# Performance work log

Measured on AMD Instinct MI355X. Metric: run time of the kernel, lower is better.

Reference implementation:

```python
import jax, jax.numpy as jnp
import numpy as np

B = 2
N_PER = 100000
M_PER = 27648
C = 32
Z, Y, X = 21, 400, 352
MAX_RANGE = (2, 2, 2)
RADIUS = 8.0
NSAMPLE = 16
VS = np.array([0.2, 0.2, 0.4], np.float32)  # voxel size (x, y, z)


def setup_inputs() -> dict:
    key = jax.random.key(0)
    ks = jax.random.split(key, 6)
    N = B * N_PER
    M = B * M_PER
    space = jnp.array([X * VS[0], Y * VS[1], Z * VS[2]], jnp.float32)
    xyz = jax.random.uniform(ks[0], (N, 3), jnp.float32) * space
    zc = jax.random.randint(ks[1], (M,), 0, Z)
    yc = jax.random.randint(ks[2], (M,), 0, Y)
    xc = jax.random.randint(ks[3], (M,), 0, X)
    bq = jnp.repeat(jnp.arange(B, dtype=jnp.int32), M_PER)
    new_coords = jnp.stack([bq, zc, yc, xc], 1).astype(jnp.int32)
    new_xyz = jnp.stack([(xc + 0.5) * VS[0], (yc + 0.5) * VS[1], (zc + 0.5) * VS[2]], 1).astype(jnp.float32)
    features = jax.random.normal(ks[4], (N, C), jnp.float32)
    raw = jax.random.randint(ks[5], (B, Z, Y, X), -N_PER, N_PER)
    offs = (jnp.arange(B) * N_PER)[:, None, None, None]
    voxel2point_indices = jnp.where(raw < 0, -1, raw + offs).astype(jnp.int32)
    xyz_batch_cnt = jnp.full((B,), N_PER, jnp.int32)
    new_xyz_batch_cnt = jnp.full((B,), M_PER, jnp.int32)
    return dict(new_coords=new_coords, xyz=xyz, xyz_batch_cnt=xyz_batch_cnt,
                new_xyz=new_xyz, new_xyz_batch_cnt=new_xyz_batch_cnt,
                features=features, voxel2point_indices=voxel2point_indices)


def _voxel_query(xyz, new_xyz, new_coords, point_indices):
    """Vectorized equivalent of the CUDA voxel_query kernel.
    Returns (idx (M, nsample) int32 global point indices, empty_ball_mask (M,) bool)."""
    zr, yr, xr = MAX_RANGE
    _, Zg, Yg, Xg = point_indices.shape
    M = new_coords.shape[0]
    dz, dy, dx = jnp.meshgrid(jnp.arange(-zr, zr + 1), jnp.arange(-yr, yr + 1),
                              jnp.arange(-xr, xr + 1), indexing='ij')
    offs = jnp.stack([dz.ravel(), dy.ravel(), dx.ravel()], 1)  # (K,3) in CUDA loop order z,y,x
    nb = new_coords[:, None, 1:4] + offs[None]                 # (M,K,3) candidate voxels
    lim = jnp.array([Zg, Yg, Xg])
    inb = jnp.all((nb >= 0) & (nb < lim), -1)                  # (M,K) in-bounds
    nbc = jnp.clip(nb, 0, lim - 1)
    b = new_coords[:, 0]
    pidx = point_indices[b[:, None], nbc[..., 0], nbc[..., 1], nbc[..., 2]]  # (M,K)
    valid = inb & (pidx >= 0)
    pts = xyz[jnp.maximum(pidx, 0)]                            # (M,K,3)
    d2 = jnp.sum((pts - new_xyz[:, None, :]) ** 2, -1)
    valid = valid & (d2 < RADIUS * RADIUS)
    cnt = jnp.minimum(valid.sum(-1), NSAMPLE)                  # (M,)
    # assign each valid candidate its in-order slot; overflow/invalid go to dump column
    slot = jnp.cumsum(valid, -1) - 1
    slot = jnp.where(valid & (slot < NSAMPLE), slot, NSAMPLE)
    rows = jnp.arange(M)[:, None]
    idx = jnp.zeros((M, NSAMPLE + 1), jnp.int32).at[rows, slot].set(pidx)[:, :NSAMPLE]
    first = idx[:, 0]  # CUDA pre-fills all slots with first found index
    idx = jnp.where(jnp.arange(NSAMPLE)[None, :] < cnt[:, None], idx, first[:, None])
    empty = cnt == 0
    idx = jnp.where(empty[:, None], 0, idx)
    return idx, empty


def reference(new_coords, xyz, xyz_batch_cnt, new_xyz, new_xyz_batch_cnt, features, voxel2point_indices):
    idx, empty = _voxel_query(xyz, new_xyz, new_coords, voxel2point_indices)
    # global -> batch-relative (as in the torch loop), empty balls -> 0 of their batch
    xyz_offs = jnp.concatenate([jnp.zeros(1, jnp.int32), jnp.cumsum(xyz_batch_cnt)[:-1].astype(jnp.int32)])
    qb = new_coords[:, 0]
    idx_rel = jnp.where(empty[:, None], 0, idx - xyz_offs[qb][:, None])
    # grouping_operation (stack version): gather with batch offset added back
    gidx = idx_rel + xyz_offs[qb][:, None]                     # (M, nsample) global indices
    grouped_xyz = jnp.transpose(xyz[gidx], (0, 2, 1))          # (M, 3, nsample)
    grouped_features = jnp.transpose(features[gidx], (0, 2, 1))  # (M, C, nsample)
    return grouped_features, grouped_xyz, empty
```

## Files before the change

kernel.cpp:

```cpp
#include <hip/hip_runtime.h>


constexpr int ZG = 21;
constexpr int YG = 400;
constexpr int XG = 352;
constexpr int NS = 16;
constexpr int CF = 32;
constexpr float R2 = 64.0f;

typedef float v4f __attribute__((ext_vector_type(4)));

__global__ __launch_bounds__(256) void pad_xyz_kernel(
    const float* __restrict__ xyz, float4* __restrict__ xyz4, int N)
{
    const int i = blockIdx.x * 256 + threadIdx.x;
    if (i < N) {
        const float* p = xyz + (size_t)i * 3;
        xyz4[i] = make_float4(p[0], p[1], p[2], 0.0f);
    }
}

template<bool USE4>
__global__ __launch_bounds__(256) void vqg_kernel(
    const int*    __restrict__ new_coords,
    const float*  __restrict__ xyz,
    const float4* __restrict__ xyz4,
    const int*    __restrict__ xyz_batch_cnt,
    const float*  __restrict__ new_xyz,
    const float*  __restrict__ features,
    const int*    __restrict__ v2p,
    float* __restrict__ out_feat,
    float* __restrict__ out_xyz,
    float* __restrict__ out_empty,
    int M)
{
    const int lane = threadIdx.x & 63;
    const int wid  = threadIdx.x >> 6;
    const int m    = blockIdx.x * 4 + wid;
    __shared__ int   sg[4][NS];
    __shared__ float tile[4][NS][33];

    const bool active = (m < M);
    int cnt  = 0;
    int boff = 0;

    if (active) {
        const int4 qc = *reinterpret_cast<const int4*>(new_coords + (size_t)m * 4);
        const int b = qc.x, zc = qc.y, yc = qc.z, xc = qc.w;
        const float qx = new_xyz[m * 3 + 0];
        const float qy = new_xyz[m * 3 + 1];
        const float qz = new_xyz[m * 3 + 2];
        for (int i = 0; i < b; ++i) boff += xyz_batch_cnt[i];
        const int* __restrict__ gb = v2p + (size_t)b * (ZG * YG * XG);

        const int n0 = lane;
        const int n1 = 64 + lane;
        int pidx0 = -1, pidx1 = -1;
        {
            const int z = zc + (n0 / 25 - 2);
            const int y = yc + ((n0 / 5) % 5 - 2);
            const int x = xc + (n0 % 5 - 2);
            if ((unsigned)z < (unsigned)ZG && (unsigned)y < (unsigned)YG &&
                (unsigned)x < (unsigned)XG)
                pidx0 = gb[((size_t)z * YG + y) * XG + x];
        }
        if (n1 < 125) {
            const int z = zc + (n1 / 25 - 2);
            const int y = yc + ((n1 / 5) % 5 - 2);
            const int x = xc + (n1 % 5 - 2);
            if ((unsigned)z < (unsigned)ZG && (unsigned)y < (unsigned)YG &&
                (unsigned)x < (unsigned)XG)
                pidx1 = gb[((size_t)z * YG + y) * XG + x];
        }

        float p0x = 0, p0y = 0, p0z = 0, p1x = 0, p1y = 0, p1z = 0;
        if (pidx0 >= 0) {
            if (USE4) {
                const float4 p = xyz4[pidx0];
                p0x = p.x; p0y = p.y; p0z = p.z;
            } else {
                p0x = xyz[(size_t)pidx0 * 3 + 0];
                p0y = xyz[(size_t)pidx0 * 3 + 1];
                p0z = xyz[(size_t)pidx0 * 3 + 2];
            }
        }
        if (pidx1 >= 0) {
            if (USE4) {
                const float4 p = xyz4[pidx1];
                p1x = p.x; p1y = p.y; p1z = p.z;
            } else {
                p1x = xyz[(size_t)pidx1 * 3 + 0];
                p1y = xyz[(size_t)pidx1 * 3 + 1];
                p1z = xyz[(size_t)pidx1 * 3 + 2];
            }
        }

        bool v0 = false, v1 = false;
        if (pidx0 >= 0) {
            const float dx = p0x - qx, dy = p0y - qy, dz = p0z - qz;
            const float d2 = __fadd_rn(__fadd_rn(__fmul_rn(dx, dx), __fmul_rn(dy, dy)),
                                       __fmul_rn(dz, dz));
            v0 = d2 < R2;
        }
        if (pidx1 >= 0) {
            const float dx = p1x - qx, dy = p1y - qy, dz = p1z - qz;
            const float d2 = __fadd_rn(__fadd_rn(__fmul_rn(dx, dx), __fmul_rn(dy, dy)),
                                       __fmul_rn(dz, dz));
            v1 = d2 < R2;
        }

        const unsigned long long below = (1ull << lane) - 1ull;
        const unsigned long long bal0 = __ballot(v0);
        const unsigned long long bal1 = __ballot(v1);
        const int c0   = (int)__popcll(bal0);
        const int pos0 = (int)__popcll(bal0 & below);
        const int pos1 = c0 + (int)__popcll(bal1 & below);
        if (v0 && pos0 < NS) sg[wid][pos0] = pidx0;
        if (v1 && pos1 < NS) sg[wid][pos1] = pidx1;
        cnt = c0 + (int)__popcll(bal1);
    }
    __syncthreads();

    if (active && lane < NS) {
        int g;
        if (cnt == 0) {
            g = boff;
        } else {
            const int c = cnt < NS ? cnt : NS;
            g = (lane < c) ? sg[wid][lane] : sg[wid][0];
        }
        sg[wid][lane] = g;
    }
    __syncthreads();

    const int K = active ? (cnt > 0 ? (cnt < NS ? cnt : NS) : 1) : 0;
    if (active) {
        const int half = lane >> 5;
        const int c    = lane & 31;
        for (int r = half; r < K; r += 2) {
            tile[wid][r][c] = features[(size_t)sg[wid][r] * CF + c];
        }
    }
    __syncthreads();

    if (active) {
        if (lane < 48) {
            const int s = lane & 15;
            const int d = lane >> 4;
            const int row = sg[wid][s];
            const float val = USE4 ? reinterpret_cast<const float*>(xyz4 + row)[d]
                                   : xyz[(size_t)row * 3 + d];
            __builtin_nontemporal_store(val, out_xyz + (size_t)m * 48 + d * 16 + s);
        }
        if (lane == 0)
            __builtin_nontemporal_store(cnt == 0 ? 1.0f : 0.0f, out_empty + m);

        float* __restrict__ of = out_feat + (size_t)m * (CF * NS);
        #pragma unroll
        for (int k = 0; k < 2; ++k) {
            const int c  = k * 16 + (lane >> 2);
            const int s0 = (lane & 3) * 4;
            v4f v;
            #pragma unroll
            for (int j = 0; j < 4; ++j) {
                const int s = s0 + j;
                v[j] = tile[wid][s < K ? s : 0][c];
            }
            __builtin_nontemporal_store(
                v, reinterpret_cast<v4f*>(of + k * 256 + (lane << 2)));
        }
    }
}

extern "C" void kernel_launch(void* const* d_in, const int* in_sizes, int n_in,
                              void* d_out, int out_size, void* d_ws, size_t ws_size,
                              hipStream_t stream) {
    const int*   new_coords    = (const int*)d_in[0];
    const float* xyz           = (const float*)d_in[1];
    const int*   xyz_batch_cnt = (const int*)d_in[2];
    const float* new_xyz       = (const float*)d_in[3];
    const float* features      = (const float*)d_in[5];
    const int*   v2p           = (const int*)d_in[6];

    const int M = in_sizes[0] / 4;
    const int N = in_sizes[1] / 3;

    float* out_feat  = (float*)d_out;
    float* out_xyz   = out_feat + (size_t)M * CF * NS;
    float* out_empty = out_xyz + (size_t)M * 3 * NS;

    const int blocks = (M + 3) / 4;
    const bool use4 = ws_size >= (size_t)N * sizeof(float4);

    if (use4) {
        float4* xyz4 = (float4*)d_ws;
        pad_xyz_kernel<<<(N + 255) / 256, 256, 0, stream>>>(xyz, xyz4, N);
        vqg_kernel<true><<<blocks, 256, 0, stream>>>(
            new_coords, xyz, xyz4, xyz_batch_cnt, new_xyz, features, v2p,
            out_feat, out_xyz, out_empty, M);
    } else {
        vqg_kernel<false><<<blocks, 256, 0, stream>>>(
            new_coords, xyz, nullptr, xyz_batch_cnt, new_xyz, features, v2p,
            out_feat, out_xyz, out_empty, M);
    }
}
```

Before: 61.85 us.

## Replace shared-memory compaction and feature tile with wave permutes and direct gathers

Neighbour-index compaction now uses ds_permute and shuffles inside each wave instead of shared-memory arrays and three __syncthreads barriers, and features are gathered straight from global memory into the vectorised output stores without an LDS tile. Each wave also exits early when it has no query. This removes block-level synchronisation and LDS traffic, at the cost of redundant global loads for repeated slot indices, which caches should absorb. The fallback path without workspace is dropped, so a large enough workspace is now assumed.

Result: no change. 61.85 us (-0.0%).

```diff
diff --git a/kernel.cpp b/kernel.cpp
--- a/kernel.cpp
+++ b/kernel.cpp
@@ -20,10 +20,8 @@
     }
 }
 
-template<bool USE4>
 __global__ __launch_bounds__(256) void vqg_kernel(
     const int*    __restrict__ new_coords,
-    const float*  __restrict__ xyz,
     const float4* __restrict__ xyz4,
     const int*    __restrict__ xyz_batch_cnt,
     const float*  __restrict__ new_xyz,
@@ -35,140 +33,105 @@
     int M)
 {
     const int lane = threadIdx.x & 63;
-    const int wid  = threadIdx.x >> 6;
-    const int m    = blockIdx.x * 4 + wid;
-    __shared__ int   sg[4][NS];
-    __shared__ float tile[4][NS][33];
+    const int m    = (blockIdx.x * 256 + threadIdx.x) >> 6;
+    if (m >= M) return;
 
-    const bool active = (m < M);
-    int cnt  = 0;
+    const int4 qc = *reinterpret_cast<const int4*>(new_coords + (size_t)m * 4);
+    const int b = qc.x, zc = qc.y, yc = qc.z, xc = qc.w;
+    const float qx = new_xyz[m * 3 + 0];
+    const float qy = new_xyz[m * 3 + 1];
+    const float qz = new_xyz[m * 3 + 2];
     int boff = 0;
+    for (int i = 0; i < b; ++i) boff += xyz_batch_cnt[i];
+    const int* __restrict__ gb = v2p + (size_t)b * (ZG * YG * XG);
 
-    if (active) {
-        const int4 qc = *reinterpret_cast<const int4*>(new_coords + (size_t)m * 4);
-        const int b = qc.x, zc = qc.y, yc = qc.z, xc = qc.w;
-        const float qx = new_xyz[m * 3 + 0];
-        const float qy = new_xyz[m * 3 + 1];
-        const float qz = new_xyz[m * 3 + 2];
-        for (int i = 0; i < b; ++i) boff += xyz_batch_cnt[i];
-        const int* __restrict__ gb = v2p + (size_t)b * (ZG * YG * XG);
+    const int n0 = lane;
+    const int n1 = 64 + lane;
+    int pidx0 = -1, pidx1 = -1;
+    {
+        const int z = zc + (n0 / 25 - 2);
+        const int y = yc + ((n0 / 5) % 5 - 2);
+        const int x = xc + (n0 % 5 - 2);
+        if ((unsigned)z < (unsigned)ZG && (unsigned)y < (unsigned)YG &&
+            (unsigned)x < (unsigned)XG)
+            pidx0 = gb[((size_t)z * YG + y) * XG + x];
+    }
+    if (n1 < 125) {
+        const int z = zc + (n1 / 25 - 2);
+        const int y = yc + ((n1 / 5) % 5 - 2);
+        const int x = xc + (n1 % 5 - 2);
+        if ((unsigned)z < (unsigned)ZG && (unsigned)y < (unsigned)YG &&
+            (unsigned)x < (unsigned)XG)
+            pidx1 = gb[((size_t)z * YG + y) * XG + x];
+    }
 
-        const int n0 = lane;
-        const int n1 = 64 + lane;
-        int pidx0 = -1, pidx1 = -1;
-        {
-            const int z = zc + (n0 / 25 - 2);
-            const int y = yc + ((n0 / 5) % 5 - 2);
-            const int x = xc + (n0 % 5 - 2);
-            if ((unsigned)z < (unsigned)ZG && (unsigned)y < (unsigned)YG &&
-                (unsigned)x < (unsigned)XG)
-                pidx0 = gb[((size_t)z * YG + y) * XG + x];
-        }
-        if (n1 < 125) {
-            const int z = zc + (n1 / 25 - 2);
-            const int y = yc + ((n1 / 5) % 5 - 2);
-            const int x = xc + (n1 % 5 - 2);
-            if ((unsigned)z < (unsigned)ZG && (unsigned)y < (unsigned)YG &&
-                (unsigned)x < (unsigned)XG)
-                pidx1 = gb[((size_t)z * YG + y) * XG + x];
-        }
+    float p0x = 0, p0y = 0, p0z = 0, p1x = 0, p1y = 0, p1z = 0;
+    if (pidx0 >= 0) {
+        const float4 p = xyz4[pidx0];
+        p0x = p.x; p0y = p.y; p0z = p.z;
+    }
+    if (pidx1 >= 0) {
+        const float4 p = xyz4[pidx1];
+        p1x = p.x; p1y = p.y; p1z = p.z;
+    }
 
-        float p0x = 0, p0y = 0, p0z = 0, p1x = 0, p1y = 0, p1z = 0;
-        if (pidx0 >= 0) {
-            if (USE4) {
-                const float4 p = xyz4[pidx0];
-                p0x = p.x; p0y = p.y; p0z = p.z;
-            } else {
-                p0x = xyz[(size_t)pidx0 * 3 + 0];
-                p0y = xyz[(size_t)pidx0 * 3 + 1];
-                p0z = xyz[(size_t)pidx0 * 3 + 2];
-            }
-        }
-        if (pidx1 >= 0) {
-            if (USE4) {
-                const float4 p = xyz4[pidx1];
-                p1x = p.x; p1y = p.y; p1z = p.z;
-            } else {
-                p1x = xyz[(size_t)pidx1 * 3 + 0];
-                p1y = xyz[(size_t)pidx1 * 3 + 1];
-                p1z = xyz[(size_t)pidx1 * 3 + 2];
-            }
-        }
+    bool v0 = false, v1 = false;
+    if (pidx0 >= 0) {
+        const float dx = p0x - qx, dy = p0y - qy, dz = p0z - qz;
+        v0 = __fadd_rn(__fadd_rn(__fmul_rn(dx, dx), __fmul_rn(dy, dy)),
+                       __fmul_rn(dz, dz)) < R2;
+    }
+    if (pidx1 >= 0) {
+        const float dx = p1x - qx, dy = p1y - qy, dz = p1z - qz;
+        v1 = __fadd_rn(__fadd_rn(__fmul_rn(dx, dx), __fmul_rn(dy, dy)),
+                       __fmul_rn(dz, dz)) < R2;
+    }
 
-        bool v0 = false, v1 = false;
-        if (pidx0 >= 0) {
-            const float dx = p0x - qx, dy = p0y - qy, dz = p0z - qz;
-            const float d2 = __fadd_rn(__fadd_rn(__fmul_rn(dx, dx), __fmul_rn(dy, dy)),
-                                       __fmul_rn(dz, dz));
-            v0 = d2 < R2;
-        }
-        if (pidx1 >= 0) {
-            const float dx = p1x - qx, dy = p1y - qy, dz = p1z - qz;
-            const float d2 = __fadd_rn(__fadd_rn(__fmul_rn(dx, dx), __fmul_rn(dy, dy)),
-                                       __fmul_rn(dz, dz));
-            v1 = d2 < R2;
-        }
+    const unsigned long long below = (1ull << lane) - 1ull;
+    const unsigned long long bal0 = __ballot(v0);
+    const unsigned long long bal1 = __ballot(v1);
+    const int c0   = (int)__popcll(bal0);
+    const int cnt  = c0 + (int)__popcll(bal1);
+    const int pos0 = (int)__popcll(bal0 & below);
+    const int pos1 = c0 + (int)__popcll(bal1 & below);
 
-        const unsigned long long below = (1ull << lane) - 1ull;
-        const unsigned long long bal0 = __ballot(v0);
-        const unsigned long long bal1 = __ballot(v1);
-        const int c0   = (int)__popcll(bal0);
-        const int pos0 = (int)__popcll(bal0 & below);
-        const int pos1 = c0 + (int)__popcll(bal1 & below);
-        if (v0 && pos0 < NS) sg[wid][pos0] = pidx0;
-        if (v1 && pos1 < NS) sg[wid][pos1] = pidx1;
-        cnt = c0 + (int)__popcll(bal1);
+    const int junk  = (16 + (lane & 31)) << 2;
+    const int addr0 = (v0 && pos0 < NS) ? (pos0 << 2) : junk;
+    const int addr1 = (v1 && pos1 < NS) ? (pos1 << 2) : junk;
+    const int perm0 = __builtin_amdgcn_ds_permute(addr0, pidx0);
+    const int perm1 = __builtin_amdgcn_ds_permute(addr1, pidx1);
+
+    const int sel   = (lane < c0) ? perm0 : perm1;
+    const int first = __shfl(sel, 0);
+    const int cnt16 = cnt < NS ? cnt : NS;
+    const int gfin  = (cnt == 0) ? boff : (((lane & 15) < cnt16) ? sel : first);
+
+    if (lane < 48) {
+        const int s = lane & 15;
+        const int d = lane >> 4;
+        const int row = __shfl(gfin, s);
+        const float val = reinterpret_cast<const float*>(xyz4 + row)[d];
+        __builtin_nontemporal_store(val, out_xyz + (size_t)m * 48 + d * 16 + s);
     }
-    __syncthreads();
+    if (lane == 0)
+        __builtin_nontemporal_store(cnt == 0 ? 1.0f : 0.0f, out_empty + m);
 
-    if (active && lane < NS) {
-        int g;
-        if (cnt == 0) {
-            g = boff;
-        } else {
-            const int c = cnt < NS ? cnt : NS;
-            g = (lane < c) ? sg[wid][lane] : sg[wid][0];
-        }
-        sg[wid][lane] = g;
-    }
-    __syncthreads();
-
-    const int K = active ? (cnt > 0 ? (cnt < NS ? cnt : NS) : 1) : 0;
-    if (active) {
-        const int half = lane >> 5;
-        const int c    = lane & 31;
-        for (int r = half; r < K; r += 2) {
-            tile[wid][r][c] = features[(size_t)sg[wid][r] * CF + c];
-        }
-    }
-    __syncthreads();
-
-    if (active) {
-        if (lane < 48) {
-            const int s = lane & 15;
-            const int d = lane >> 4;
-            const int row = sg[wid][s];
-            const float val = USE4 ? reinterpret_cast<const float*>(xyz4 + row)[d]
-                                   : xyz[(size_t)row * 3 + d];
-            __builtin_nontemporal_store(val, out_xyz + (size_t)m * 48 + d * 16 + s);
-        }
-        if (lane == 0)
-            __builtin_nontemporal_store(cnt == 0 ? 1.0f : 0.0f, out_empty + m);
-
-        float* __restrict__ of = out_feat + (size_t)m * (CF * NS);
-        #pragma unroll
-        for (int k = 0; k < 2; ++k) {
-            const int c  = k * 16 + (lane >> 2);
-            const int s0 = (lane & 3) * 4;
-            v4f v;
-            #pragma unroll
-            for (int j = 0; j < 4; ++j) {
-                const int s = s0 + j;
-                v[j] = tile[wid][s < K ? s : 0][c];
-            }
-            __builtin_nontemporal_store(
-                v, reinterpret_cast<v4f*>(of + k * 256 + (lane << 2)));
-        }
+    const int s0 = (lane & 3) << 2;
+    const int r0 = __shfl(gfin, s0 + 0);
+    const int r1 = __shfl(gfin, s0 + 1);
+    const int r2 = __shfl(gfin, s0 + 2);
+    const int r3 = __shfl(gfin, s0 + 3);
+    float* __restrict__ of = out_feat + (size_t)m * (CF * NS);
+    #pragma unroll
+    for (int k = 0; k < 2; ++k) {
+        const int c = k * 16 + (lane >> 2);
+        v4f v;
+        v[0] = features[(size_t)r0 * CF + c];
+        v[1] = features[(size_t)r1 * CF + c];
+        v[2] = features[(size_t)r2 * CF + c];
+        v[3] = features[(size_t)r3 * CF + c];
+        __builtin_nontemporal_store(
+            v, reinterpret_cast<v4f*>(of + k * 256 + (lane << 2)));
     }
 }
 
@@ -189,18 +152,11 @@
     float* out_xyz   = out_feat + (size_t)M * CF * NS;
     float* out_empty = out_xyz + (size_t)M * 3 * NS;
 
+    float4* xyz4 = (float4*)d_ws;
+    pad_xyz_kernel<<<(N + 255) / 256, 256, 0, stream>>>(xyz, xyz4, N);
+
     const int blocks = (M + 3) / 4;
-    const bool use4 = ws_size >= (size_t)N * sizeof(float4);
-
-    if (use4) {
-        float4* xyz4 = (float4*)d_ws;
-        pad_xyz_kernel<<<(N + 255) / 256, 256, 0, stream>>>(xyz, xyz4, N);
-        vqg_kernel<true><<<blocks, 256, 0, stream>>>(
-            new_coords, xyz, xyz4, xyz_batch_cnt, new_xyz, features, v2p,
-            out_feat, out_xyz, out_empty, M);
-    } else {
-        vqg_kernel<false><<<blocks, 256, 0, stream>>>(
-            new_coords, xyz, nullptr, xyz_batch_cnt, new_xyz, features, v2p,
-            out_feat, out_xyz, out_empty, M);
-    }
+    vqg_kernel<<<blocks, 256, 0, stream>>>(
+        new_coords, xyz4, xyz_batch_cnt, new_xyz, features, v2p,
+        out_feat, out_xyz, out_empty, M);
 }
```
